# Kernel tuning notes

Hardware: AMD Instinct MI355X
Metric: run time of the kernel (lower is better)

Reference implementation:

```python
import jax, jax.numpy as jnp
import numpy as np

B, T, C, H = 4, 2048, 1024, 16  # batch, seq, d_model, heads
D = C // H                      # head_dim = 64


def setup_inputs() -> dict:
    key = jax.random.key(0)
    ks = jax.random.split(key, 7)
    s = 1.0 / np.sqrt(C)
    return {
        "q_x": jax.random.normal(ks[0], (B, T, C), jnp.float32),
        "Wq": jax.random.normal(ks[1], (C, C), jnp.float32) * s,
        "bq": jax.random.normal(ks[2], (C,), jnp.float32) * 0.01,
        "Wk": jax.random.normal(ks[3], (C, C), jnp.float32) * s,
        "bk": jax.random.normal(ks[4], (C,), jnp.float32) * 0.01,
        "Wv": jax.random.normal(ks[5], (C, C), jnp.float32) * s,
        "bv": jax.random.normal(ks[6], (C,), jnp.float32) * 0.01,
    }


def reference(q_x, Wq, bq, Wk, bk, Wv, bv):
    # Self-attention path (k_x = v_x = q_x). Torch Linear: y = x @ W.T + b.
    q = q_x @ Wq.T + bq          # [B,T,C]
    k = q_x @ Wk.T + bk
    v = q_x @ Wv.T + bv
    # split heads: (B,T,C) -> (B,H,T,D); matches torch reshape(T,B*H,D) layout
    def heads(x):
        return x.reshape(B, T, H, D).transpose(0, 2, 1, 3)
    qh, kh, vh = heads(q), heads(k), heads(v)
    scale = 1.0 / np.sqrt(D)
    attn = jnp.einsum('bhtd,bhsd->bhts', qh, kh) * scale  # [B,H,T,T]
    attn = jax.nn.softmax(attn, axis=-1)
    x = jnp.einsum('bhts,bhsd->bhtd', attn, vh)           # [B,H,T,D]
    # merge heads back -> (B,T,C); batch_first=True output
    return x.transpose(0, 2, 1, 3).reshape(B, T, C)
```

## Files before the change

### kernel.cpp

```cpp
#include <hip/hip_runtime.h>
#include <hip/hip_bf16.h>
#include <stdint.h>
#include <stddef.h>

#define B_ 4
#define T_ 2048
#define C_ 1024
#define H_ 16
#define D_ 64
#define M_ (B_ * T_)

typedef __bf16 bf16x8 __attribute__((ext_vector_type(8)));
typedef float  f32x4  __attribute__((ext_vector_type(4)));
typedef unsigned short u16x8 __attribute__((ext_vector_type(8)));
typedef unsigned short u16x4 __attribute__((ext_vector_type(4)));
typedef unsigned int   u32x4 __attribute__((ext_vector_type(4)));

__device__ __forceinline__ unsigned short f2bf(float f) {
    union { float f; unsigned int u; } c; c.f = f;
    unsigned int u = c.u;
    unsigned int r = (u + 0x7fffu + ((u >> 16) & 1u)) >> 16;
    return (unsigned short)r;
}

__device__ __forceinline__ unsigned int pack2bf(float a, float b) {
    unsigned int ua = __builtin_bit_cast(unsigned int, a) + 0x8000u;
    unsigned int ub = __builtin_bit_cast(unsigned int, b) + 0x8000u;
    return __builtin_amdgcn_perm(ub, ua, 0x07060302u);
}

__device__ __forceinline__ bf16x8 ld_bf16x8(const unsigned short* p) {
    u16x8 v = *(const u16x8*)p;
    return __builtin_bit_cast(bf16x8, v);
}

__device__ __forceinline__ void gl_lds16(const unsigned short* g, unsigned short* l) {
    __builtin_amdgcn_global_load_lds(
        (const void __attribute__((address_space(1)))*)g,
        (void __attribute__((address_space(3)))*)l, 16, 0, 0);
}

__device__ __forceinline__ f32x4 vmax4(f32x4 a, f32x4 b) {
    f32x4 r;
    r.x = fmaxf(a.x, b.x); r.y = fmaxf(a.y, b.y);
    r.z = fmaxf(a.z, b.z); r.w = fmaxf(a.w, b.w);
    return r;
}

#define X4_ ((int64_t)M_ * C_ / 4)
#define W4_ ((int64_t)C_ * C_ / 4)

__global__ __launch_bounds__(256)
void cvt_bf16(const float* __restrict__ x,
              const float* __restrict__ Wq, const float* __restrict__ Wk,
              const float* __restrict__ Wv,
              unsigned short* __restrict__ xb, unsigned short* __restrict__ wb)
{
    const int64_t i4 = (int64_t)blockIdx.x * blockDim.x + threadIdx.x;
    const float* src; unsigned short* dst; int64_t off;
    if (i4 < X4_) { src = x; dst = xb; off = i4; }
    else {
        int64_t j = i4 - X4_;
        int which = (int)(j / W4_);
        off = j - (int64_t)which * W4_;
        src = (which == 0) ? Wq : (which == 1) ? Wk : Wv;
        dst = wb + (int64_t)which * C_ * C_;
    }
    f32x4 v = *(const f32x4*)(src + off * 4);
    u16x4 o = { f2bf(v.x), f2bf(v.y), f2bf(v.z), f2bf(v.w) };
    *(u16x4*)(dst + off * 4) = o;
}

#define K1_ 0.180336880f

__global__ __launch_bounds__(256)
void qkv_gemm(const unsigned short* __restrict__ xb,
              const unsigned short* __restrict__ wb,
              const float* __restrict__ bq, const float* __restrict__ bk,
              const float* __restrict__ bv,
              unsigned short* __restrict__ qo,
              unsigned short* __restrict__ ko,
              unsigned short* __restrict__ vo)
{
    __shared__ alignas(16) unsigned short As[128 * 64];
    __shared__ alignas(16) unsigned short Bs[128 * 64];

    const int tid   = threadIdx.x;
    const int bm    = blockIdx.x;
    const int bn    = blockIdx.y;
    const int which = bn >> 3;
    const int n_base = (bn & 7) * 128;
    const int nrow   = bn * 128;
    const int m_base = bm * 128;

    const float* bias = (which == 0) ? bq : (which == 1) ? bk : bv;

    const int w = tid >> 6, lane = tid & 63;
    const int wr = w >> 1, wc = w & 1;
    const int ln = lane & 15, quad = lane >> 4;

    const int srow   = lane >> 3;
    const int schunk = (lane & 7) ^ srow;
    const int scu    = schunk * 8;

    const f32x4 fz = {0.f, 0.f, 0.f, 0.f};
    f32x4 acc[4][4];
#pragma unroll
    for (int i = 0; i < 4; ++i)
#pragma unroll
        for (int j = 0; j < 4; ++j) acc[i][j] = fz;

    for (int k0 = 0; k0 < C_; k0 += 64) {
        __syncthreads();
#pragma unroll
        for (int i = 0; i < 4; ++i) {
            const int r = w * 32 + i * 8 + srow;
            gl_lds16(xb + (size_t)(m_base + r) * C_ + k0 + scu, As + (w * 4 + i) * 512);
            gl_lds16(wb + (size_t)(nrow  + r) * C_ + k0 + scu, Bs + (w * 4 + i) * 512);
        }
        __syncthreads();

#pragma unroll
        for (int kk = 0; kk < 2; ++kk) {
            bf16x8 af[4], bfr[4];
#pragma unroll
            for (int mi = 0; mi < 4; ++mi) {
                const int r = wr * 64 + mi * 16 + ln;
                af[mi] = ld_bf16x8(&As[r * 64 + (((kk * 4 + quad) ^ (ln & 7)) * 8)]);
            }
#pragma unroll
            for (int ni = 0; ni < 4; ++ni) {
                const int r = wc * 64 + ni * 16 + ln;
                bfr[ni] = ld_bf16x8(&Bs[r * 64 + (((kk * 4 + quad) ^ (ln & 7)) * 8)]);
            }
#pragma unroll
            for (int mi = 0; mi < 4; ++mi)
#pragma unroll
                for (int ni = 0; ni < 4; ++ni)
                    acc[mi][ni] = __builtin_amdgcn_mfma_f32_16x16x32_bf16(
                        af[mi], bfr[ni], acc[mi][ni], 0, 0, 0);
        }
    }

#pragma unroll
    for (int ni = 0; ni < 4; ++ni) {
        const int n_local = n_base + wc * 64 + ni * 16 + ln;
        const float bv_ = bias[n_local];
        const int h = n_local >> 6, d = n_local & 63;
#pragma unroll
        for (int mi = 0; mi < 4; ++mi) {
            const int m0 = m_base + wr * 64 + mi * 16 + quad * 4;
            const int b  = m0 >> 11;
            const int t0 = m0 & (T_ - 1);
            f32x4 v = acc[mi][ni];
            if (which == 2) {
                const int tb   = t0 & ~127;
                const int w128 = t0 & 127;
                const int kvt  = w128 >> 4;
                const int qd   = (w128 >> 2) & 3;
                const int pos  = (kvt >> 1) * 32 + qd * 8 + (kvt & 1) * 4;
                u16x4 pk = { f2bf(v.x + bv_), f2bf(v.y + bv_),
                             f2bf(v.z + bv_), f2bf(v.w + bv_) };
                *(u16x4*)(&vo[((size_t)(b * H_ + h) * D_ + d) * T_ + tb + pos]) = pk;
            } else if (which == 0) {
                unsigned short* dst =
                    qo + ((size_t)(b * H_ + h) * T_ + t0) * (size_t)D_ + d;
                dst[0 * D_] = f2bf((v.x + bv_) * K1_);
                dst[1 * D_] = f2bf((v.y + bv_) * K1_);
                dst[2 * D_] = f2bf((v.z + bv_) * K1_);
                dst[3 * D_] = f2bf((v.w + bv_) * K1_);
            } else {
                unsigned short* dst =
                    ko + ((size_t)(b * H_ + h) * T_ + t0) * (size_t)D_ + d;
                dst[0 * D_] = f2bf(v.x + bv_);
                dst[1 * D_] = f2bf(v.y + bv_);
                dst[2 * D_] = f2bf(v.z + bv_);
                dst[3 * D_] = f2bf(v.w + bv_);
            }
        }
    }
}

__global__ __launch_bounds__(256)
void flash_attn(const unsigned short* __restrict__ qb,
                const unsigned short* __restrict__ kb,
                const unsigned short* __restrict__ vtb,
                float* __restrict__ out)
{
    __shared__ alignas(16) unsigned char smem[49152];
    float* Os = (float*)smem;
    unsigned short* Vs = (unsigned short*)(smem + 32768);

    const int tid = threadIdx.x;
    const int qt  = blockIdx.x;
    const int bh  = blockIdx.y;
    const int b   = bh >> 4, h = bh & 15;

    const int w = tid >> 6, lane = tid & 63;
    const int ln = lane & 15, quad = lane >> 4;

    const unsigned short* Qb = qb  + (size_t)bh * T_ * D_;
    const unsigned short* Kb = kb  + (size_t)bh * T_ * D_;
    const unsigned short* Vb = vtb + (size_t)bh * D_ * T_;

    const int qrow0 = qt * 128 + w * 16 + ln;
    const bf16x8 qA0 = ld_bf16x8(&Qb[(size_t)qrow0 * D_ + quad * 8]);
    const bf16x8 qA1 = ld_bf16x8(&Qb[(size_t)qrow0 * D_ + 32 + quad * 8]);
    const bf16x8 qB0 = ld_bf16x8(&Qb[(size_t)(qrow0 + 64) * D_ + quad * 8]);
    const bf16x8 qB1 = ld_bf16x8(&Qb[(size_t)(qrow0 + 64) * D_ + 32 + quad * 8]);

    const int srow   = lane >> 3;
    const int schunk = (lane & 7) ^ srow;
    const int scu    = schunk * 8;
    const int vrow = lane >> 4;

    const f32x4 fz = {0.f, 0.f, 0.f, 0.f};
    float m2a = -3.0e38f, lia = 0.f;
    float m2b = -3.0e38f, lib = 0.f;
    f32x4 accA[4], accB[4];
#pragma unroll
    for (int dt = 0; dt < 4; ++dt) { accA[dt] = fz; accB[dt] = fz; }

    auto stageK = [&](int kv0, int buf) {
        unsigned short* Ks = (unsigned short*)(smem + buf * 16384);
#pragma unroll
        for (int i = 0; i < 4; ++i) {
            const int kr = kv0 + w * 32 + i * 8 + srow;
            gl_lds16(Kb + (size_t)kr * D_ + scu, Ks + (w * 4 + i) * 512);
        }
    };
    auto stageV = [&](int kv0) {
#pragma unroll
        for (int i = 0; i < 4; ++i) {
            const int dr = (w * 4 + i) * 4 + vrow;
            const int vcs = (lane & 15) ^ ((i & 1) * 4 + vrow);
            gl_lds16(Vb + (size_t)dr * T_ + kv0 + vcs * 8, Vs + (w * 4 + i) * 512);
        }
    };

    stageK(0, 0);

    for (int kv0 = 0; kv0 < T_; kv0 += 128) {
        const int cur = (kv0 >> 7) & 1;
        __syncthreads();
        stageV(kv0);
        if (kv0 + 128 < T_) stageK(kv0 + 128, cur ^ 1);

        const unsigned short* Ks = (const unsigned short*)(smem + cur * 16384);

        f32x4 sA[8], sB[8];
#pragma unroll
        for (int kvt = 0; kvt < 8; ++kvt) {
            const int r_ = kvt * 16 + ln;
            bf16x8 kf0 = ld_bf16x8(&Ks[r_ * 64 + ((quad)     ^ (ln & 7)) * 8]);
            bf16x8 kf1 = ld_bf16x8(&Ks[r_ * 64 + ((quad + 4) ^ (ln & 7)) * 8]);
            f32x4 cA = fz, cB = fz;
            cA = __builtin_amdgcn_mfma_f32_16x16x32_bf16(kf0, qA0, cA, 0, 0, 0);
            cB = __builtin_amdgcn_mfma_f32_16x16x32_bf16(kf0, qB0, cB, 0, 0, 0);
            cA = __builtin_amdgcn_mfma_f32_16x16x32_bf16(kf1, qA1, cA, 0, 0, 0);
            cB = __builtin_amdgcn_mfma_f32_16x16x32_bf16(kf1, qB1, cB, 0, 0, 0);
            sA[kvt] = cA; sB[kvt] = cB;
        }

        u32x4 pksA[4], pksB[4];
        float alA, alB;
        {
            f32x4 mm = vmax4(vmax4(vmax4(sA[0], sA[1]), vmax4(sA[2], sA[3])),
                             vmax4(vmax4(sA[4], sA[5]), vmax4(sA[6], sA[7])));
            float mx = fmaxf(fmaxf(mm.x, mm.y), fmaxf(mm.z, mm.w));
            mx = fmaxf(mx, __shfl_xor(mx, 16));
            mx = fmaxf(mx, __shfl_xor(mx, 32));
            const float nm = fmaxf(m2a, mx);
            alA = __builtin_amdgcn_exp2f(m2a - nm);
            m2a = nm;
            f32x4 rsv = fz;
#pragma unroll
            for (int p = 0; p < 4; ++p) {
                f32x4 e0, e1;
                e0.x = __builtin_amdgcn_exp2f(sA[2*p].x - m2a);
                e0.y = __builtin_amdgcn_exp2f(sA[2*p].y - m2a);
                e0.z = __builtin_amdgcn_exp2f(sA[2*p].z - m2a);
                e0.w = __builtin_amdgcn_exp2f(sA[2*p].w - m2a);
                e1.x = __builtin_amdgcn_exp2f(sA[2*p+1].x - m2a);
                e1.y = __builtin_amdgcn_exp2f(sA[2*p+1].y - m2a);
                e1.z = __builtin_amdgcn_exp2f(sA[2*p+1].z - m2a);
                e1.w = __builtin_amdgcn_exp2f(sA[2*p+1].w - m2a);
                rsv += e0; rsv += e1;
                pksA[p][0] = pack2bf(e0.x, e0.y);
                pksA[p][1] = pack2bf(e0.z, e0.w);
                pksA[p][2] = pack2bf(e1.x, e1.y);
                pksA[p][3] = pack2bf(e1.z, e1.w);
            }
            float rs = (rsv.x + rsv.y) + (rsv.z + rsv.w);
            rs += __shfl_xor(rs, 16);
            rs += __shfl_xor(rs, 32);
            lia = lia * alA + rs;
        }
        {
            f32x4 mm = vmax4(vmax4(vmax4(sB[0], sB[1]), vmax4(sB[2], sB[3])),
                             vmax4(vmax4(sB[4], sB[5]), vmax4(sB[6], sB[7])));
            float mx = fmaxf(fmaxf(mm.x, mm.y), fmaxf(mm.z, mm.w));
            mx = fmaxf(mx, __shfl_xor(mx, 16));
            mx = fmaxf(mx, __shfl_xor(mx, 32));
            const float nm = fmaxf(m2b, mx);
            alB = __builtin_amdgcn_exp2f(m2b - nm);
            m2b = nm;
            f32x4 rsv = fz;
#pragma unroll
            for (int p = 0; p < 4; ++p) {
                f32x4 e0, e1;
                e0.x = __builtin_amdgcn_exp2f(sB[2*p].x - m2b);
                e0.y = __builtin_amdgcn_exp2f(sB[2*p].y - m2b);
                e0.z = __builtin_amdgcn_exp2f(sB[2*p].z - m2b);
                e0.w = __builtin_amdgcn_exp2f(sB[2*p].w - m2b);
                e1.x = __builtin_amdgcn_exp2f(sB[2*p+1].x - m2b);
                e1.y = __builtin_amdgcn_exp2f(sB[2*p+1].y - m2b);
                e1.z = __builtin_amdgcn_exp2f(sB[2*p+1].z - m2b);
                e1.w = __builtin_amdgcn_exp2f(sB[2*p+1].w - m2b);
                rsv += e0; rsv += e1;
                pksB[p][0] = pack2bf(e0.x, e0.y);
                pksB[p][1] = pack2bf(e0.z, e0.w);
                pksB[p][2] = pack2bf(e1.x, e1.y);
                pksB[p][3] = pack2bf(e1.z, e1.w);
            }
            float rs = (rsv.x + rsv.y) + (rsv.z + rsv.w);
            rs += __shfl_xor(rs, 16);
            rs += __shfl_xor(rs, 32);
            lib = lib * alB + rs;
        }

#pragma unroll
        for (int dt = 0; dt < 4; ++dt) { accA[dt] *= alA; accB[dt] *= alB; }

        __syncthreads();

#pragma unroll
        for (int dt = 0; dt < 4; ++dt) {
            const int vr = dt * 16 + ln;
#pragma unroll
            for (int p = 0; p < 4; ++p) {
                const int cl = ((p * 4 + quad) ^ (ln & 7));
                bf16x8 vv = ld_bf16x8(&Vs[vr * 128 + cl * 8]);
                accA[dt] = __builtin_amdgcn_mfma_f32_16x16x32_bf16(
                    vv, __builtin_bit_cast(bf16x8, pksA[p]), accA[dt], 0, 0, 0);
                accB[dt] = __builtin_amdgcn_mfma_f32_16x16x32_bf16(
                    vv, __builtin_bit_cast(bf16x8, pksB[p]), accB[dt], 0, 0, 0);
            }
        }
    }

    __syncthreads();
    const float rva = 1.0f / lia, rvb = 1.0f / lib;
#pragma unroll
    for (int dt = 0; dt < 4; ++dt)
#pragma unroll
        for (int r = 0; r < 4; ++r) {
            Os[(w * 16 + ln) * 72 + dt * 16 + quad * 4 + r]        = accA[dt][r] * rva;
            Os[(64 + w * 16 + ln) * 72 + dt * 16 + quad * 4 + r]   = accB[dt][r] * rvb;
        }
    __syncthreads();

    const int q  = tid >> 1;
    const int c0 = (tid & 1) * 32;
    const float* src = &Os[q * 72 + c0];
    float* dst = &out[((size_t)(b * T_ + qt * 128 + q)) * C_ + h * 64 + c0];
#pragma unroll
    for (int i = 0; i < 8; ++i)
        *(f32x4*)(dst + i * 4) = *(const f32x4*)(src + i * 4);
}

extern "C" void kernel_launch(void* const* d_in, const int* in_sizes, int n_in,
                              void* d_out, int out_size, void* d_ws, size_t ws_size,
                              hipStream_t stream) {
    const float* q_x = (const float*)d_in[0];
    const float* Wq  = (const float*)d_in[1];
    const float* bq  = (const float*)d_in[2];
    const float* Wk  = (const float*)d_in[3];
    const float* bk  = (const float*)d_in[4];
    const float* Wv  = (const float*)d_in[5];
    const float* bv  = (const float*)d_in[6];
    float* out = (float*)d_out;

    const size_t elems = (size_t)M_ * C_;
    unsigned short* xb  = (unsigned short*)d_ws;
    unsigned short* wb  = xb + elems;
    unsigned short* qb  = wb + (size_t)3 * C_ * C_;
    unsigned short* kb  = qb + elems;
    unsigned short* vtb = kb + elems;
    (void)ws_size; (void)in_sizes; (void)n_in; (void)out_size;

    const int64_t total4 = X4_ + 3 * W4_;
    cvt_bf16<<<(int)(total4 / 256), 256, 0, stream>>>(q_x, Wq, Wk, Wv, xb, wb);

    qkv_gemm<<<dim3(M_ / 128, 24), 256, 0, stream>>>(
        xb, wb, bq, bk, bv, qb, kb, vtb);

    flash_attn<<<dim3(T_ / 128, B_ * H_), 256, 0, stream>>>(qb, kb, vtb, out);
}
```

Measured before the change: 274.3 us.

## Read V directly from global memory and remap attention blocks across XCDs

Removes V staging through LDS. Each wave now loads its V fragments straight from global memory, which drops one barrier per KV tile and shrinks shared memory. The 2D grid becomes a flat 1024-block grid with an index swizzle, so that blocks sharing a (batch, head) land on the same XCD. The kernel also asks for two blocks per SM via launch bounds. The trade-off is that every wave now does redundant global/L2 reads of V, with none of the LDS reuse across waves, which could raise memory traffic.

Result: slower. 354.4 us (+29.2%).

```diff
diff --git a/kernel.cpp b/kernel.cpp
--- a/kernel.cpp
+++ b/kernel.cpp
@@ -181,20 +181,21 @@
     }
 }
 
-__global__ __launch_bounds__(256)
+__global__ __launch_bounds__(256, 2)
 void flash_attn(const unsigned short* __restrict__ qb,
                 const unsigned short* __restrict__ kb,
                 const unsigned short* __restrict__ vtb,
                 float* __restrict__ out)
 {
-    __shared__ alignas(16) unsigned char smem[49152];
+    __shared__ alignas(16) unsigned char smem[36864];
     float* Os = (float*)smem;
-    unsigned short* Vs = (unsigned short*)(smem + 32768);
 
     const int tid = threadIdx.x;
-    const int qt  = blockIdx.x;
-    const int bh  = blockIdx.y;
-    const int b   = bh >> 4, h = bh & 15;
+    const int flat = blockIdx.x;
+    const int tile = (flat & 7) * 128 + (flat >> 3);
+    const int qt   = tile & 15;
+    const int bh   = tile >> 4;
+    const int b    = bh >> 4, h = bh & 15;
 
     const int w = tid >> 6, lane = tid & 63;
     const int ln = lane & 15, quad = lane >> 4;
@@ -212,7 +213,6 @@
     const int srow   = lane >> 3;
     const int schunk = (lane & 7) ^ srow;
     const int scu    = schunk * 8;
-    const int vrow = lane >> 4;
 
     const f32x4 fz = {0.f, 0.f, 0.f, 0.f};
     float m2a = -3.0e38f, lia = 0.f;
@@ -221,20 +221,12 @@
 #pragma unroll
     for (int dt = 0; dt < 4; ++dt) { accA[dt] = fz; accB[dt] = fz; }
 
-    auto stageK = [&](int kv0, int buf) {
+    auto stageK = [&](int kv0_, int buf) {
         unsigned short* Ks = (unsigned short*)(smem + buf * 16384);
 #pragma unroll
         for (int i = 0; i < 4; ++i) {
-            const int kr = kv0 + w * 32 + i * 8 + srow;
+            const int kr = kv0_ + w * 32 + i * 8 + srow;
             gl_lds16(Kb + (size_t)kr * D_ + scu, Ks + (w * 4 + i) * 512);
-        }
-    };
-    auto stageV = [&](int kv0) {
-#pragma unroll
-        for (int i = 0; i < 4; ++i) {
-            const int dr = (w * 4 + i) * 4 + vrow;
-            const int vcs = (lane & 15) ^ ((i & 1) * 4 + vrow);
-            gl_lds16(Vb + (size_t)dr * T_ + kv0 + vcs * 8, Vs + (w * 4 + i) * 512);
         }
     };
 
@@ -243,7 +235,6 @@
     for (int kv0 = 0; kv0 < T_; kv0 += 128) {
         const int cur = (kv0 >> 7) & 1;
         __syncthreads();
-        stageV(kv0);
         if (kv0 + 128 < T_) stageK(kv0 + 128, cur ^ 1);
 
         const unsigned short* Ks = (const unsigned short*)(smem + cur * 16384);
@@ -332,15 +323,12 @@
 #pragma unroll
         for (int dt = 0; dt < 4; ++dt) { accA[dt] *= alA; accB[dt] *= alB; }
 
-        __syncthreads();
-
 #pragma unroll
         for (int dt = 0; dt < 4; ++dt) {
-            const int vr = dt * 16 + ln;
+            const unsigned short* vp = Vb + (size_t)(dt * 16 + ln) * T_ + kv0;
 #pragma unroll
             for (int p = 0; p < 4; ++p) {
-                const int cl = ((p * 4 + quad) ^ (ln & 7));
-                bf16x8 vv = ld_bf16x8(&Vs[vr * 128 + cl * 8]);
+                bf16x8 vv = ld_bf16x8(&vp[(p * 4 + quad) * 8]);
                 accA[dt] = __builtin_amdgcn_mfma_f32_16x16x32_bf16(
                     vv, __builtin_bit_cast(bf16x8, pksA[p]), accA[dt], 0, 0, 0);
                 accB[dt] = __builtin_amdgcn_mfma_f32_16x16x32_bf16(
@@ -395,5 +383,5 @@
     qkv_gemm<<<dim3(M_ / 128, 24), 256, 0, stream>>>(
         xb, wb, bq, bk, bv, qb, kb, vtb);
 
-    flash_attn<<<dim3(T_ / 128, B_ * H_), 256, 0, stream>>>(qb, kb, vtb, out);
-}
+    flash_attn<<<1024, 256, 0, stream>>>(qb, kb, vtb, out);
+}
```
